# Kernel tuning notes

Hardware: AMD Instinct MI355X
Metric: run time of the kernel (lower is better)

The kernel has to match this reference:

```python
import jax, jax.numpy as jnp
import numpy as np

EPS = 1e-12  # matches torch F.normalize default eps
WEIGHT = jnp.array([1.0, 1.0, 1.0], dtype=jnp.float32)  # per-channel loss weights


def _l2norm(x, axis):
    # torch F.normalize: x / max(||x||_2, eps)
    n = jnp.sqrt(jnp.sum(x * x, axis=axis, keepdims=True))
    return x / jnp.maximum(n, EPS)


def setup_inputs() -> dict:
    key = jax.random.key(0)
    k1, k2 = jax.random.split(key)
    shape = (16, 3, 512, 512)  # [B, C, H, W]
    return {
        "x": jax.random.normal(k1, shape, dtype=jnp.float32),
        "ref": jax.random.normal(k2, shape, dtype=jnp.float32),
    }


def reference(x, ref):
    # trace(rownorm(A) @ rownorm(B)^T) == sum(rownorm(A) * rownorm(B));
    # trace(colnorm(A)^T @ colnorm(B)) == sum(colnorm(A) * colnorm(B)).
    B, C, H, W = x.shape
    # per (batch, channel) traces, vectorized over all dims
    a = jnp.sum(_l2norm(x, -1) * _l2norm(ref, -1), axis=(-2, -1)) / H  # [B, C]
    b = jnp.sum(_l2norm(x, -2) * _l2norm(ref, -2), axis=(-2, -1)) / W  # [B, C]
    a = -jnp.sum(a * WEIGHT) / B
    b = -jnp.sum(b * WEIGHT) / B
    return a + b
```

## Files before the change

kernel.cpp:

```cpp
#include <hip/hip_runtime.h>

#define B_N 16
#define C_N 3
#define H_N 512
#define W_N 512
#define PLANES (B_N * C_N)
#define ROWS_PER_BLOCK 32
#define ROWS_PER_WAVE 8
#define CHUNKS (H_N / ROWS_PER_BLOCK)
#define NBLK (PLANES * CHUNKS)
#define STATS3 (W_N * 3)
#define SCALE (-1.0f / 8192.0f)
#define EPS_F 1e-12f

__global__ __launch_bounds__(256) void spl_main_kernel(
    const float* __restrict__ x, const float* __restrict__ r,
    float* __restrict__ colpart, float* __restrict__ rowpart) {
    const int p     = blockIdx.x / CHUNKS;
    const int chunk = blockIdx.x % CHUNKS;
    const int wave  = threadIdx.x >> 6;
    const int lane  = threadIdx.x & 63;

    const float* xp = x + (size_t)p * (H_N * W_N);
    const float* rp = r + (size_t)p * (H_N * W_N);

    float cxx[8] = {0, 0, 0, 0, 0, 0, 0, 0};
    float crr[8] = {0, 0, 0, 0, 0, 0, 0, 0};
    float cxr[8] = {0, 0, 0, 0, 0, 0, 0, 0};
    float psxx[ROWS_PER_WAVE], psrr[ROWS_PER_WAVE], psxr[ROWS_PER_WAVE];

    const int r0 = chunk * ROWS_PER_BLOCK;
    #pragma unroll
    for (int b = 0; b < 2; ++b) {
        #pragma unroll
        for (int j = 0; j < 4; ++j) {
            const int row = r0 + b * 16 + wave * 4 + j;
            const int jj = b * 4 + j;
            const float4* xr4 = (const float4*)(xp + (size_t)row * W_N);
            const float4* rr4 = (const float4*)(rp + (size_t)row * W_N);
            const float4 xa = xr4[lane];
            const float4 xb = xr4[lane + 64];
            const float4 ra = rr4[lane];
            const float4 rb = rr4[lane + 64];

            const float ax[8] = {xa.x, xa.y, xa.z, xa.w, xb.x, xb.y, xb.z, xb.w};
            const float rx[8] = {ra.x, ra.y, ra.z, ra.w, rb.x, rb.y, rb.z, rb.w};

            float sxx = 0.0f, srr = 0.0f, sxr = 0.0f;
            #pragma unroll
            for (int k = 0; k < 8; ++k) {
                const float txx = ax[k] * ax[k];
                const float trr = rx[k] * rx[k];
                const float txr = ax[k] * rx[k];
                cxx[k] += txx; crr[k] += trr; cxr[k] += txr;
                sxx += txx;    srr += trr;    sxr += txr;
            }
            psxx[jj] = sxx; psrr[jj] = srr; psxr[jj] = sxr;
        }
    }

    #pragma unroll
    for (int m = 32; m > 0; m >>= 1) {
        #pragma unroll
        for (int j = 0; j < ROWS_PER_WAVE; ++j) {
            psxx[j] += __shfl_down(psxx[j], m, 64);
            psrr[j] += __shfl_down(psrr[j], m, 64);
            psxr[j] += __shfl_down(psxr[j], m, 64);
        }
    }
    float rowacc = 0.0f;
    if (lane == 0) {
        #pragma unroll
        for (int j = 0; j < ROWS_PER_WAVE; ++j) {
            const float nx = fmaxf(sqrtf(psxx[j]), EPS_F);
            const float nr = fmaxf(sqrtf(psrr[j]), EPS_F);
            rowacc += psxr[j] / (nx * nr);
        }
    }

    __shared__ float smem[4][3][W_N];
    *(float4*)&smem[wave][0][4 * lane]       = make_float4(cxx[0], cxx[1], cxx[2], cxx[3]);
    *(float4*)&smem[wave][0][4 * lane + 256] = make_float4(cxx[4], cxx[5], cxx[6], cxx[7]);
    *(float4*)&smem[wave][1][4 * lane]       = make_float4(crr[0], crr[1], crr[2], crr[3]);
    *(float4*)&smem[wave][1][4 * lane + 256] = make_float4(crr[4], crr[5], crr[6], crr[7]);
    *(float4*)&smem[wave][2][4 * lane]       = make_float4(cxr[0], cxr[1], cxr[2], cxr[3]);
    *(float4*)&smem[wave][2][4 * lane + 256] = make_float4(cxr[4], cxr[5], cxr[6], cxr[7]);
    __shared__ float rowsums[4];
    if (lane == 0) rowsums[wave] = rowacc;
    __syncthreads();

    float* cp = colpart + (size_t)blockIdx.x * STATS3;
    #pragma unroll
    for (int k = 0; k < 6; ++k) {
        const int e = threadIdx.x + 256 * k;
        cp[e] = smem[0][0][e] + smem[1][0][e] + smem[2][0][e] + smem[3][0][e];
    }
    if (threadIdx.x == 0)
        rowpart[blockIdx.x] = rowsums[0] + rowsums[1] + rowsums[2] + rowsums[3];
}

__global__ __launch_bounds__(256) void spl_reduce_kernel(
    const float* __restrict__ colpart, const float* __restrict__ rowpart,
    float* __restrict__ planesum) {
    const int p = blockIdx.x;
    float acc[6] = {0, 0, 0, 0, 0, 0};
    const float* base = colpart + (size_t)p * CHUNKS * STATS3;
    for (int c = 0; c < CHUNKS; ++c) {
        const float* bc = base + c * STATS3;
        #pragma unroll
        for (int k = 0; k < 6; ++k) acc[k] += bc[threadIdx.x + 256 * k];
    }
    __shared__ float sums[STATS3];
    #pragma unroll
    for (int k = 0; k < 6; ++k) sums[threadIdx.x + 256 * k] = acc[k];
    __syncthreads();

    float term = 0.0f;
    #pragma unroll
    for (int k = 0; k < 2; ++k) {
        const int col = threadIdx.x + 256 * k;
        const float sxx = sums[col];
        const float srr = sums[512 + col];
        const float sxr = sums[1024 + col];
        term += sxr / (fmaxf(sqrtf(sxx), EPS_F) * fmaxf(sqrtf(srr), EPS_F));
    }
    if (threadIdx.x < CHUNKS) term += rowpart[p * CHUNKS + threadIdx.x];

    #pragma unroll
    for (int m = 32; m > 0; m >>= 1) term += __shfl_down(term, m, 64);
    __shared__ float ws[4];
    if ((threadIdx.x & 63) == 0) ws[threadIdx.x >> 6] = term;
    __syncthreads();
    if (threadIdx.x == 0) planesum[p] = ws[0] + ws[1] + ws[2] + ws[3];
}

__global__ void spl_final_kernel(const float* __restrict__ planesum,
                                 float* __restrict__ out) {
    float v = (threadIdx.x < PLANES) ? planesum[threadIdx.x] : 0.0f;
    #pragma unroll
    for (int m = 32; m > 0; m >>= 1) v += __shfl_down(v, m, 64);
    if (threadIdx.x == 0) out[0] = SCALE * v;
}

extern "C" void kernel_launch(void* const* d_in, const int* in_sizes, int n_in,
                              void* d_out, int out_size, void* d_ws, size_t ws_size,
                              hipStream_t stream) {
    const float* x   = (const float*)d_in[0];
    const float* ref = (const float*)d_in[1];
    float* out = (float*)d_out;

    float* colpart  = (float*)d_ws;
    float* rowpart  = colpart + (size_t)NBLK * STATS3;
    float* planesum = rowpart + NBLK;

    spl_main_kernel<<<NBLK, 256, 0, stream>>>(x, ref, colpart, rowpart);
    spl_reduce_kernel<<<PLANES, 256, 0, stream>>>(colpart, rowpart, planesum);
    spl_final_kernel<<<1, 64, 0, stream>>>(planesum, out);
}
```

Baseline: 120.4 us.

## Fuse main, reduce and final kernels via last-block atomic tickets

Merges the three kernel launches into one kernel. The last block to finish each plane, detected with an atomic counter, does that plane's column reduction, and the last plane-finisher does the final sum. This removes two launch gaps and the separate tail kernels, at the cost of a memset launch, threadfences and atomics, plus a serialized reduction tail inside the last blocks.

Result: slower. 192.5 us (+59.9%).

```diff
diff --git a/kernel.cpp b/kernel.cpp
--- a/kernel.cpp
+++ b/kernel.cpp
@@ -13,9 +13,11 @@
 #define SCALE (-1.0f / 8192.0f)
 #define EPS_F 1e-12f
 
-__global__ __launch_bounds__(256) void spl_main_kernel(
+__global__ __launch_bounds__(256) void spl_fused_kernel(
     const float* __restrict__ x, const float* __restrict__ r,
-    float* __restrict__ colpart, float* __restrict__ rowpart) {
+    float* __restrict__ colpart, float* __restrict__ rowpart,
+    float* __restrict__ planesum, int* __restrict__ cnt,
+    int* __restrict__ ticket, float* __restrict__ out) {
     const int p     = blockIdx.x / CHUNKS;
     const int chunk = blockIdx.x % CHUNKS;
     const int wave  = threadIdx.x >> 6;
@@ -97,12 +99,17 @@
     }
     if (threadIdx.x == 0)
         rowpart[blockIdx.x] = rowsums[0] + rowsums[1] + rowsums[2] + rowsums[3];
-}
 
-__global__ __launch_bounds__(256) void spl_reduce_kernel(
-    const float* __restrict__ colpart, const float* __restrict__ rowpart,
-    float* __restrict__ planesum) {
-    const int p = blockIdx.x;
+    __shared__ int flag;
+    __syncthreads();
+    if (threadIdx.x == 0) {
+        __threadfence();
+        flag = (atomicAdd(&cnt[p], 1) == CHUNKS - 1);
+    }
+    __syncthreads();
+    if (!flag) return;
+    __threadfence();
+
     float acc[6] = {0, 0, 0, 0, 0, 0};
     const float* base = colpart + (size_t)p * CHUNKS * STATS3;
     for (int c = 0; c < CHUNKS; ++c) {
@@ -119,27 +126,32 @@
     #pragma unroll
     for (int k = 0; k < 2; ++k) {
         const int col = threadIdx.x + 256 * k;
-        const float sxx = sums[col];
-        const float srr = sums[512 + col];
-        const float sxr = sums[1024 + col];
-        term += sxr / (fmaxf(sqrtf(sxx), EPS_F) * fmaxf(sqrtf(srr), EPS_F));
+        term += sums[1024 + col] /
+                (fmaxf(sqrtf(sums[col]), EPS_F) * fmaxf(sqrtf(sums[512 + col]), EPS_F));
     }
     if (threadIdx.x < CHUNKS) term += rowpart[p * CHUNKS + threadIdx.x];
 
     #pragma unroll
     for (int m = 32; m > 0; m >>= 1) term += __shfl_down(term, m, 64);
-    __shared__ float ws[4];
-    if ((threadIdx.x & 63) == 0) ws[threadIdx.x >> 6] = term;
+    __shared__ float ws4[4];
+    if (lane == 0) ws4[wave] = term;
     __syncthreads();
-    if (threadIdx.x == 0) planesum[p] = ws[0] + ws[1] + ws[2] + ws[3];
-}
 
-__global__ void spl_final_kernel(const float* __restrict__ planesum,
-                                 float* __restrict__ out) {
-    float v = (threadIdx.x < PLANES) ? planesum[threadIdx.x] : 0.0f;
-    #pragma unroll
-    for (int m = 32; m > 0; m >>= 1) v += __shfl_down(v, m, 64);
-    if (threadIdx.x == 0) out[0] = SCALE * v;
+    if (threadIdx.x == 0) {
+        planesum[p] = ws4[0] + ws4[1] + ws4[2] + ws4[3];
+        __threadfence();
+        flag = (atomicAdd(ticket, 1) == PLANES - 1);
+    }
+    __syncthreads();
+    if (!flag) return;
+    __threadfence();
+
+    if (threadIdx.x < 64) {
+        float v = (threadIdx.x < PLANES) ? planesum[threadIdx.x] : 0.0f;
+        #pragma unroll
+        for (int m = 32; m > 0; m >>= 1) v += __shfl_down(v, m, 64);
+        if (threadIdx.x == 0) out[0] = SCALE * v;
+    }
 }
 
 extern "C" void kernel_launch(void* const* d_in, const int* in_sizes, int n_in,
@@ -152,8 +164,10 @@
     float* colpart  = (float*)d_ws;
     float* rowpart  = colpart + (size_t)NBLK * STATS3;
     float* planesum = rowpart + NBLK;
+    int*   cnt      = (int*)(planesum + PLANES);
+    int*   ticket   = cnt + PLANES;
 
-    spl_main_kernel<<<NBLK, 256, 0, stream>>>(x, ref, colpart, rowpart);
-    spl_reduce_kernel<<<PLANES, 256, 0, stream>>>(colpart, rowpart, planesum);
-    spl_final_kernel<<<1, 64, 0, stream>>>(planesum, out);
+    hipMemsetAsync(cnt, 0, (PLANES + 1) * sizeof(int), stream);
+    spl_fused_kernel<<<NBLK, 256, 0, stream>>>(x, ref, colpart, rowpart,
+                                               planesum, cnt, ticket, out);
 }
```
